# Performance work log

Measured on AMD Instinct MI355X. Metric: run time of the kernel, lower is better.

## Reference

```python
import math
import jax, jax.numpy as jnp
import numpy as np

HID = 4096      # hidden_size
NH = 32         # num_attention_heads
HD = HID // NH  # head_dim = 128
EDGE = 24       # image_edge
K = 12          # pool_kernel_size
PE = 1 + EDGE - K  # pooled_edge = 13
VT = EDGE * EDGE   # vision_tokens = 576
OFF = 5         # image token offset
SR = 2          # scale_ratio


def setup_inputs() -> dict:
    key = jax.random.key(0)
    k1, k2, k3 = jax.random.split(key, 3)
    B, S = 2, 1024
    hidden_states = jax.random.normal(k1, (B, S, HID), jnp.float32)
    W_in = jax.random.normal(k2, (HID, HID), jnp.float32) * 0.02   # input_proj.weight [out,in]
    W_up = jax.random.normal(k3, (HD * SR * SR, HD), jnp.float32) * 0.02  # up_proj.weight [out,in]
    return {"hidden_states": hidden_states, "W_in": W_in, "W_up": W_up}


def reference(hidden_states, W_in, W_up):
    B, S, _ = hidden_states.shape
    residual = hidden_states
    # [B, NH, S, HD] (q and k are identical views of hidden_states)
    qk = hidden_states.reshape(B, S, NH, HD).transpose(0, 2, 1, 3)
    attn = jnp.einsum('bhqd,bhkd->bhqk', qk, qk) / math.sqrt(HD)
    # additive mask applied along the QUERY dim (faithful to original broadcast)
    mask = jnp.zeros((S,), attn.dtype).at[OFF:OFF + VT].set(jnp.finfo(attn.dtype).min)
    attn = attn + mask[None, None, :, None]
    attn = jax.nn.softmax(attn.astype(jnp.float32), axis=-1).astype(qk.dtype)
    attn = attn.sum(axis=2)                        # [B, NH, S]
    image_attn = attn[:, :, OFF:OFF + VT]          # [B, NH, 576]
    image_states = qk[:, :, OFF:OFF + VT, :].reshape(B, NH, EDGE, EDGE, HD)
    ia_soft = jax.nn.softmax(image_attn, axis=-1).reshape(B, NH, EDGE, EDGE)
    ia = image_attn.reshape(B, NH, EDGE, EDGE)
    # AvgPool2d(kernel=12, stride=1) -> [B, NH, 13, 13]
    pooled = jax.lax.reduce_window(ia, 0.0, jax.lax.add,
                                   (1, 1, K, K), (1, 1, 1, 1), 'VALID') / (K * K)
    idx = jnp.argmax(pooled.reshape(B, NH, -1), axis=-1)   # [B, NH]
    row = idx // PE
    col = idx % PE

    def per_head(sm, st, r, c):
        w = jax.lax.dynamic_slice(sm, (r, c), (K, K)).sum()
        win = jax.lax.dynamic_slice(st, (r, c, 0), (K, K, HD))
        return w, win

    # vmap over batch and heads; traced dynamic-slice starts replace the python loops
    w, win = jax.vmap(jax.vmap(per_head))(ia_soft, image_states, row, col)
    up = jnp.einsum('bhijd,ed->bhije', win, W_up)
    # pixel-shuffle back to 24x24 (transpose(3,4) in torch view order)
    up = up.reshape(B, NH, K, K, SR, SR, HD).transpose(0, 1, 2, 4, 3, 5, 6)
    up = up.reshape(B, NH, VT, HD) * w[:, :, None, None]
    img = up.transpose(0, 2, 1, 3).reshape(B, VT, HID)
    hs = jnp.concatenate([hidden_states[:, :OFF], img, hidden_states[:, OFF + VT:]], axis=1)
    hs = jax.nn.silu(hs @ W_in.T)
    return residual + hs
```

## Files before the change

kernel.cpp:

```cpp
#include <hip/hip_runtime.h>
#include <hip/hip_bf16.h>
#include <math.h>

#define HID 4096
#define NH 32
#define HD 128
#define EDGE 24
#define KW 12
#define PEW 13
#define VT 576
#define OFF 5
#define NB 2
#define SLEN 1024
#define QT 64
#define NQT 7
#define KT 64
#define NKT 16

typedef short bf16x8 __attribute__((ext_vector_type(8)));
typedef float f32x4 __attribute__((ext_vector_type(4)));
typedef unsigned int u32;

static __device__ __forceinline__ unsigned short f2bf(float f) {
  union { float f; u32 u; } v; v.f = f;
  u32 u = v.u;
  return (unsigned short)((u + 0x7fffu + ((u >> 16) & 1u)) >> 16);
}

static __device__ __forceinline__ float dot4(float4 a, float4 b) {
  return a.x * b.x + a.y * b.y + a.z * b.z + a.w * b.w;
}

static __device__ __forceinline__ void load_lds16(const void* g, void* l) {
  __builtin_amdgcn_global_load_lds((const __attribute__((address_space(1))) u32*)g,
                                   (__attribute__((address_space(3))) u32*)l, 16, 0, 0);
}

__global__ __launch_bounds__(256) void k_cvt(const float* __restrict__ in,
                                             unsigned short* __restrict__ out, int n4) {
  int i = blockIdx.x * 256 + threadIdx.x;
  if (i < n4) {
    float4 v = ((const float4*)in)[i];
    ushort4 o;
    o.x = f2bf(v.x); o.y = f2bf(v.y); o.z = f2bf(v.z); o.w = f2bf(v.w);
    ((ushort4*)out)[i] = o;
  }
}

__global__ __launch_bounds__(256) void k_pack(const float* __restrict__ hid,
                                              unsigned short* __restrict__ Phi,
                                              unsigned short* __restrict__ Plo) {
  int i = blockIdx.x * 256 + threadIdx.x;
  float4 x = ((const float4*)hid)[i];
  float e[4] = {x.x, x.y, x.z, x.w};
  ushort4 hv, lv;
  unsigned short* hp = (unsigned short*)&hv;
  unsigned short* lp = (unsigned short*)&lv;
#pragma unroll
  for (int j = 0; j < 4; ++j) {
    u32 u = __float_as_uint(e[j]);
    u32 hb = (u + 0x7fffu + ((u >> 16) & 1u)) >> 16;
    float r = e[j] - __uint_as_float(hb << 16);
    u32 ur = __float_as_uint(r);
    u32 lb = (ur + 0x7fffu + ((ur >> 16) & 1u)) >> 16;
    hp[j] = (unsigned short)hb;
    lp[j] = (unsigned short)lb;
  }
  ((ushort4*)Phi)[i] = hv;
  ((ushort4*)Plo)[i] = lv;
}

__global__ __launch_bounds__(512, 2) void k_scores(const unsigned short* __restrict__ Phi,
                                                   const unsigned short* __restrict__ Plo,
                                                   float* __restrict__ part) {
  __shared__ unsigned short Kh[3][KT * HD];
  __shared__ unsigned short Kl[3][KT * HD];
  __shared__ float cs[4][SLEN];
  __shared__ float zbuf[2][QT];

  int bid = blockIdx.x;
  int xcd = bid & 7, idx = bid >> 3;
  int bh = xcd * 8 + idx / NQT;
  int qt = idx % NQT;
  int b = bh >> 5, h = bh & 31;
  int t = threadIdx.x, l = t & 63, wv = t >> 6;
  int wq = wv >> 1, wk = wv & 1;

  const unsigned short* PhB = Phi + (size_t)b * SLEN * HID + h * HD;
  const unsigned short* PlB = Plo + (size_t)b * SLEN * HID + h * HD;

  bf16x8 qhi[4], qlo[4];
  {
    int ql = qt * QT + wq * 16 + (l & 15);
    int qg = (ql < OFF) ? ql : ql + VT;
    const unsigned short* ph = PhB + (size_t)qg * HID + (l >> 4) * 8;
    const unsigned short* pl = PlB + (size_t)qg * HID + (l >> 4) * 8;
#pragma unroll
    for (int ds = 0; ds < 4; ++ds) {
      qhi[ds] = *(const bf16x8*)(ph + ds * 32);
      qlo[ds] = *(const bf16x8*)(pl + ds * 32);
    }
  }

  int g0 = t, g1 = t + 512;
  int r0 = g0 >> 4, r1 = g1 >> 4;
  size_t soff0 = (size_t)r0 * HID + ((g0 & 15) ^ (r0 & 7)) * 8;
  size_t soff1 = (size_t)r1 * HID + ((g1 & 15) ^ (r1 & 7)) * 8;

#define STAGE(kt_, bb_)                                                        \
  do {                                                                         \
    size_t kb_ = (size_t)(kt_)*KT * HID;                                       \
    load_lds16(PhB + kb_ + soff0, &Kh[bb_][g0 * 8]);                           \
    load_lds16(PhB + kb_ + soff1, &Kh[bb_][g1 * 8]);                           \
    load_lds16(PlB + kb_ + soff0, &Kl[bb_][g0 * 8]);                           \
    load_lds16(PlB + kb_ + soff1, &Kl[bb_][g1 * 8]);                           \
  } while (0)

  const float scale = 0.088388347648318447f;

  int foff[2][4];
#pragma unroll
  for (int c = 0; c < 2; ++c) {
    int rb = wk * 32 + c * 16 + (l & 15);
#pragma unroll
    for (int ds = 0; ds < 4; ++ds)
      foff[c][ds] = rb * HD + (((ds * 4) + (l >> 4)) ^ (rb & 7)) * 8;
  }

  float e[NKT][2][4];

  STAGE(0, 0);
  STAGE(1, 1);

#pragma unroll
  for (int tt = 0; tt < NKT; ++tt) {
    int bb = tt % 3;
    if (tt < NKT - 1) {
      asm volatile("s_waitcnt vmcnt(4)" ::: "memory");
    } else {
      asm volatile("s_waitcnt vmcnt(0)" ::: "memory");
    }
    __builtin_amdgcn_s_barrier();
    __builtin_amdgcn_sched_barrier(0);

    bf16x8 kh[2][4], kl[2][4];
#pragma unroll
    for (int c = 0; c < 2; ++c)
#pragma unroll
      for (int ds = 0; ds < 4; ++ds) {
        kh[c][ds] = *(const bf16x8*)&Kh[bb][foff[c][ds]];
        kl[c][ds] = *(const bf16x8*)&Kl[bb][foff[c][ds]];
      }
    if (tt + 2 < NKT) STAGE(tt + 2, (tt + 2) % 3);

#pragma unroll
    for (int c = 0; c < 2; ++c) {
      f32x4 aP = {0.f, 0.f, 0.f, 0.f};
      f32x4 aQ = {0.f, 0.f, 0.f, 0.f};
      f32x4 aR = {0.f, 0.f, 0.f, 0.f};
#pragma unroll
      for (int ds = 0; ds < 4; ++ds) {
        aP = __builtin_amdgcn_mfma_f32_16x16x32_bf16(qhi[ds], kh[c][ds], aP, 0, 0, 0);
        aQ = __builtin_amdgcn_mfma_f32_16x16x32_bf16(qhi[ds], kl[c][ds], aQ, 0, 0, 0);
        aR = __builtin_amdgcn_mfma_f32_16x16x32_bf16(qlo[ds], kh[c][ds], aR, 0, 0, 0);
      }
#pragma unroll
      for (int jj = 0; jj < 4; ++jj)
        e[tt][c][jj] = __expf((aP[jj] + aQ[jj] + aR[jj]) * scale);
    }
  }
#undef STAGE

  float zr[4] = {0.f, 0.f, 0.f, 0.f};
#pragma unroll
  for (int tt = 0; tt < NKT; ++tt)
#pragma unroll
    for (int c = 0; c < 2; ++c)
#pragma unroll
      for (int jj = 0; jj < 4; ++jj) zr[jj] += e[tt][c][jj];
#pragma unroll
  for (int jj = 0; jj < 4; ++jj) {
    float z = zr[jj];
    z += __shfl_xor(z, 1);
    z += __shfl_xor(z, 2);
    z += __shfl_xor(z, 4);
    z += __shfl_xor(z, 8);
    zr[jj] = z;
  }
  if ((l & 15) == 0) {
#pragma unroll
    for (int jj = 0; jj < 4; ++jj)
      zbuf[wk][wq * 16 + (l >> 4) * 4 + jj] = zr[jj];
  }
  __syncthreads();

  float zinv[4];
#pragma unroll
  for (int jj = 0; jj < 4; ++jj) {
    int row = wq * 16 + (l >> 4) * 4 + jj;
    zinv[jj] = 1.f / (zbuf[0][row] + zbuf[1][row]);
  }

#pragma unroll
  for (int tt = 0; tt < NKT; ++tt)
#pragma unroll
    for (int c = 0; c < 2; ++c) {
      float v = e[tt][c][0] * zinv[0] + e[tt][c][1] * zinv[1] +
                e[tt][c][2] * zinv[2] + e[tt][c][3] * zinv[3];
      v += __shfl_xor(v, 16);
      v += __shfl_xor(v, 32);
      if (l < 16) cs[wq][tt * KT + wk * 32 + c * 16 + l] = v;
    }
  __syncthreads();

  for (int c5 = t; c5 < VT; c5 += 512) {
    int col = OFF + c5;
    part[((size_t)bh * NQT + qt) * VT + c5] =
        (cs[0][col] + cs[1][col]) + (cs[2][col] + cs[3][col]);
  }
}

__global__ __launch_bounds__(256) void k_head(const float* __restrict__ part,
                                              float* __restrict__ params) {
  int bh = blockIdx.x;
  int t = threadIdx.x;
  __shared__ float ia[VT];
  __shared__ float sfe[VT];
  __shared__ float rbuf[256];
  __shared__ int ribuf[256];

  for (int i = t; i < VT; i += 256) {
    float s = 0.f;
    const float* p = part + (size_t)bh * NQT * VT + i;
    for (int c = 0; c < NQT; ++c) s += p[(size_t)c * VT];
    ia[i] = s;
  }
  __syncthreads();

  float lm = -1e30f;
  for (int i = t; i < VT; i += 256) lm = fmaxf(lm, ia[i]);
  rbuf[t] = lm;
  __syncthreads();
  for (int s = 128; s > 0; s >>= 1) {
    if (t < s) rbuf[t] = fmaxf(rbuf[t], rbuf[t + s]);
    __syncthreads();
  }
  float M = rbuf[0];
  __syncthreads();

  float lz = 0.f;
  for (int i = t; i < VT; i += 256) {
    float e = __expf(ia[i] - M);
    sfe[i] = e;
    lz += e;
  }
  rbuf[t] = lz;
  __syncthreads();
  for (int s = 128; s > 0; s >>= 1) {
    if (t < s) rbuf[t] += rbuf[t + s];
    __syncthreads();
  }
  float invZ = 1.f / rbuf[0];
  __syncthreads();

  float pv = -1e30f;
  int pidx = 0x7fffffff;
  if (t < PEW * PEW) {
    int r = t / PEW, c = t % PEW;
    float s = 0.f;
    for (int i = 0; i < KW; ++i)
      for (int j = 0; j < KW; ++j) s += ia[(r + i) * EDGE + (c + j)];
    pv = s;
    pidx = t;
  }
  rbuf[t] = pv;
  ribuf[t] = pidx;
  __syncthreads();
  for (int s = 128; s > 0; s >>= 1) {
    if (t < s) {
      float ov = rbuf[t + s];
      int oi = ribuf[t + s];
      if (ov > rbuf[t] || (ov == rbuf[t] && oi < ribuf[t])) {
        rbuf[t] = ov;
        ribuf[t] = oi;
      }
    }
    __syncthreads();
  }
  int idx = ribuf[0];
  int r0 = idx / PEW, c0 = idx % PEW;
  __syncthreads();

  float lw = 0.f;
  if (t < KW * KW) {
    int i = t / KW, j = t % KW;
    lw = sfe[(r0 + i) * EDGE + (c0 + j)];
  }
  rbuf[t] = lw;
  __syncthreads();
  for (int s = 128; s > 0; s >>= 1) {
    if (t < s) rbuf[t] += rbuf[t + s];
    __syncthreads();
  }
  if (t == 0) {
    params[bh * 4 + 0] = rbuf[0] * invZ;
    ((int*)params)[bh * 4 + 1] = r0;
    ((int*)params)[bh * 4 + 2] = c0;
  }
}

__global__ __launch_bounds__(256) void k_img(const float* __restrict__ hid,
                                             const float* __restrict__ Wup,
                                             const float* __restrict__ params,
                                             unsigned short* __restrict__ hs) {
  int bid = blockIdx.x;
  int g = bid & 3;
  int bh = bid >> 2;
  int b = bh / NH, h = bh % NH;
  float w = params[bh * 4];
  int r0 = ((const int*)params)[bh * 4 + 1];
  int c0 = ((const int*)params)[bh * 4 + 2];
  int t = threadIdx.x;

  __shared__ float win[36][HD];
  for (int idx = t; idx < 36 * (HD / 4); idx += 256) {
    int cell = idx >> 5;
    int c4 = idx & 31;
    int cc = g * 36 + cell;
    int i = cc / 12, j = cc % 12;
    int s = OFF + (r0 + i) * EDGE + (c0 + j);
    *(float4*)&win[cell][c4 * 4] =
        *(const float4*)(hid + ((size_t)(b * SLEN + s)) * HID + h * HD + c4 * 4);
  }
  __syncthreads();

  float acc0[36], acc1[36];
#pragma unroll
  for (int cell = 0; cell < 36; ++cell) { acc0[cell] = 0.f; acc1[cell] = 0.f; }

  int e0 = t, e1 = t + 256;
  const float* w0 = Wup + (size_t)e0 * HD;
  const float* w1 = Wup + (size_t)e1 * HD;
  for (int c = 0; c < 32; ++c) {
    float4 u0 = *(const float4*)(w0 + c * 4);
    float4 u1 = *(const float4*)(w1 + c * 4);
#pragma unroll
    for (int cell = 0; cell < 36; ++cell) {
      float4 qv = *(const float4*)&win[cell][c * 4];
      acc0[cell] += dot4(qv, u0);
      acc1[cell] += dot4(qv, u1);
    }
  }

  int si0 = e0 >> 8, sj0 = (e0 >> 7) & 1, d0 = e0 & 127;
  int si1 = e1 >> 8, sj1 = (e1 >> 7) & 1, d1 = e1 & 127;
#pragma unroll
  for (int cell = 0; cell < 36; ++cell) {
    int cc = g * 36 + cell;
    int i = cc / 12, j = cc % 12;
    {
      int srow = OFF + (2 * i + si0) * EDGE + (2 * j + sj0);
      hs[((size_t)(b * SLEN + srow)) * HID + h * HD + d0] = f2bf(acc0[cell] * w);
    }
    {
      int srow = OFF + (2 * i + si1) * EDGE + (2 * j + sj1);
      hs[((size_t)(b * SLEN + srow)) * HID + h * HD + d1] = f2bf(acc1[cell] * w);
    }
  }
}

__global__ __launch_bounds__(512, 2) void k_gemm(const unsigned short* __restrict__ A,
                                                 const unsigned short* __restrict__ Bm,
                                                 const float* __restrict__ resid,
                                                 float* __restrict__ out) {
  __shared__ unsigned short lA[3][128 * 64];
  __shared__ unsigned short lB[3][256 * 64];

  int bid0 = blockIdx.x;
  int swz = (bid0 & 7) * 32 + (bid0 >> 3);
  int bm0 = (swz & 15) << 7;
  int bn0 = (swz >> 4) << 8;
  int t = threadIdx.x;
  int ln = t & 63, wv = t >> 6;
  int wr = wv >> 2, wc = wv & 3;

  int aOff[4][2], bOff[4][2];
#pragma unroll
  for (int q = 0; q < 4; ++q)
#pragma unroll
    for (int ks = 0; ks < 2; ++ks) {
      int ga = ks * 4 + (ln >> 4);
      int ra = wr * 64 + q * 16 + (ln & 15);
      aOff[q][ks] = ra * 64 + ((ga ^ (ra & 7)) * 8);
      int rb = wc * 64 + q * 16 + (ln & 15);
      bOff[q][ks] = rb * 64 + ((ga ^ (rb & 7)) * 8);
    }

  const unsigned short* aS0; const unsigned short* aS1;
  unsigned short *aD0, *aD1;
  {
    int G = t, r = G >> 3, g = G & 7;
    aS0 = A + (size_t)(bm0 + r) * HID + ((g ^ (r & 7)) * 8);
    aD0 = &lA[0][0] + G * 8;
    G = t + 512; r = G >> 3; g = G & 7;
    aS1 = A + (size_t)(bm0 + r) * HID + ((g ^ (r & 7)) * 8);
    aD1 = &lA[0][0] + G * 8;
  }
  const unsigned short *bS0, *bS1, *bS2, *bS3;
  unsigned short *bD0, *bD1, *bD2, *bD3;
  {
    int G = t, r = G >> 3, g = G & 7;
    bS0 = Bm + (size_t)(bn0 + r) * HID + ((g ^ (r & 7)) * 8);
    bD0 = &lB[0][0] + G * 8;
    G = t + 512; r = G >> 3; g = G & 7;
    bS1 = Bm + (size_t)(bn0 + r) * HID + ((g ^ (r & 7)) * 8);
    bD1 = &lB[0][0] + G * 8;
    G = t + 1024; r = G >> 3; g = G & 7;
    bS2 = Bm + (size_t)(bn0 + r) * HID + ((g ^ (r & 7)) * 8);
    bD2 = &lB[0][0] + G * 8;
    G = t + 1536; r = G >> 3; g = G & 7;
    bS3 = Bm + (size_t)(bn0 + r) * HID + ((g ^ (r & 7)) * 8);
    bD3 = &lB[0][0] + G * 8;
  }

#define STAGE_ALL(kt_, nb_)                                \
  load_lds16(aS0 + (kt_) * 64, aD0 + (nb_) * 8192);        \
  load_lds16(aS1 + (kt_) * 64, aD1 + (nb_) * 8192);        \
  load_lds16(bS0 + (kt_) * 64, bD0 + (nb_) * 16384);       \
  load_lds16(bS1 + (kt_) * 64, bD1 + (nb_) * 16384);       \
  load_lds16(bS2 + (kt_) * 64, bD2 + (nb_) * 16384);       \
  load_lds16(bS3 + (kt_) * 64, bD3 + (nb_) * 16384);

  f32x4 acc[4][4];
#pragma unroll
  for (int mi = 0; mi < 4; ++mi)
#pragma unroll
    for (int ni = 0; ni < 4; ++ni) acc[mi][ni] = (f32x4){0.f, 0.f, 0.f, 0.f};

  STAGE_ALL(0, 0);
  STAGE_ALL(1, 1);

  int cur = 0;
  for (int kt = 0; kt < 64; ++kt) {
    if (kt < 63) {
      asm volatile("s_waitcnt vmcnt(6)" ::: "memory");
    } else {
      asm volatile("s_waitcnt vmcnt(0)" ::: "memory");
    }
    __builtin_amdgcn_s_barrier();
    __builtin_amdgcn_sched_barrier(0);

    const unsigned short* Ab = &lA[0][0] + cur * 8192;
    const unsigned short* Bb = &lB[0][0] + cur * 16384;

    bf16x8 aF[4][2], bF[4][2];
#pragma unroll
    for (int q = 0; q < 4; ++q) {
      aF[q][0] = *(const bf16x8*)(Ab + aOff[q][0]);
      aF[q][1] = *(const bf16x8*)(Ab + aOff[q][1]);
      bF[q][0] = *(const bf16x8*)(Bb + bOff[q][0]);
      bF[q][1] = *(const bf16x8*)(Bb + bOff[q][1]);
    }

    int nb = cur + 2; if (nb >= 3) nb -= 3;
    if (kt < 62) { STAGE_ALL(kt + 2, nb); }

    __builtin_amdgcn_s_setprio(1);
#pragma unroll
    for (int ni = 0; ni < 4; ++ni)
#pragma unroll
      for (int mi = 0; mi < 4; ++mi) {
        acc[mi][ni] = __builtin_amdgcn_mfma_f32_16x16x32_bf16(aF[mi][0], bF[ni][0],
                                                              acc[mi][ni], 0, 0, 0);
        acc[mi][ni] = __builtin_amdgcn_mfma_f32_16x16x32_bf16(aF[mi][1], bF[ni][1],
                                                              acc[mi][ni], 0, 0, 0);
      }
    __builtin_amdgcn_s_setprio(0);

    cur = cur + 1; if (cur >= 3) cur = 0;
  }
#undef STAGE_ALL

#pragma unroll
  for (int mi = 0; mi < 4; ++mi) {
#pragma unroll
    for (int ni = 0; ni < 4; ++ni) {
      int m = bm0 + wr * 64 + mi * 16 + (ln >> 4) * 4;
      int n = bn0 + wc * 64 + ni * 16 + (ln & 15);
#pragma unroll
      for (int r = 0; r < 4; ++r) {
        float x = acc[mi][ni][r];
        float s = x / (1.f + __expf(-x));
        size_t o = (size_t)(m + r) * HID + n;
        out[o] = resid[o] + s;
      }
    }
  }
}

extern "C" void kernel_launch(void* const* d_in, const int* in_sizes, int n_in,
                              void* d_out, int out_size, void* d_ws, size_t ws_size,
                              hipStream_t stream) {
  const float* hid = (const float*)d_in[0];
  const float* Win = (const float*)d_in[1];
  const float* Wup = (const float*)d_in[2];
  float* out = (float*)d_out;
  char* ws = (char*)d_ws;

  unsigned short* Wb  = (unsigned short*)ws;
  unsigned short* Phi = (unsigned short*)(ws + 33554432);
  float* part = (float*)(ws + 50331648);
  float* params = (float*)(ws + 52396032);
  unsigned short* Plo = (unsigned short*)d_out;

  k_cvt<<<16384, 256, 0, stream>>>(Win, Wb, HID * HID / 4);
  k_pack<<<NB * SLEN * HID / 4 / 256, 256, 0, stream>>>(hid, Phi, Plo);
  k_scores<<<448, 512, 0, stream>>>(Phi, Plo, part);
  k_head<<<NB * NH, 256, 0, stream>>>(part, params);
  k_img<<<NB * NH * 4, 256, 0, stream>>>(hid, Wup, params, Phi);
  k_gemm<<<256, 512, 0, stream>>>(Phi, Wb, hid, out);
}
```

Measured before the change: 193.6 us.

## Fuse fp32 weight conversion into GEMM loads and switch to 32x32 MFMA

Removes the separate W_in fp32-to-bf16 conversion kernel. The GEMM now loads fp32 weight rows into registers, converts them, and writes swizzled bf16 into LDS one stage ahead, double-buffered through register sets. The MFMA tiling also moves from 16x16x32 to 32x32x16 instructions, with new fragment offsets and epilogue indexing. This saves a full pass over the 64MB weight, but each of the 8 M-tile blocks sharing a weight tile now re-reads it in fp32, doubling weight traffic inside the GEMM and adding VALU conversion and register pressure to the main loop.

```diff
diff --git a/kernel.cpp b/kernel.cpp
--- a/kernel.cpp
+++ b/kernel.cpp
@@ -19,6 +19,7 @@
 
 typedef short bf16x8 __attribute__((ext_vector_type(8)));
 typedef float f32x4 __attribute__((ext_vector_type(4)));
+typedef float f32x16 __attribute__((ext_vector_type(16)));
 typedef unsigned int u32;
 
 static __device__ __forceinline__ unsigned short f2bf(float f) {
@@ -34,17 +35,6 @@
 static __device__ __forceinline__ void load_lds16(const void* g, void* l) {
   __builtin_amdgcn_global_load_lds((const __attribute__((address_space(1))) u32*)g,
                                    (__attribute__((address_space(3))) u32*)l, 16, 0, 0);
-}
-
-__global__ __launch_bounds__(256) void k_cvt(const float* __restrict__ in,
-                                             unsigned short* __restrict__ out, int n4) {
-  int i = blockIdx.x * 256 + threadIdx.x;
-  if (i < n4) {
-    float4 v = ((const float4*)in)[i];
-    ushort4 o;
-    o.x = f2bf(v.x); o.y = f2bf(v.y); o.z = f2bf(v.z); o.w = f2bf(v.w);
-    ((ushort4*)out)[i] = o;
-  }
 }
 
 __global__ __launch_bounds__(256) void k_pack(const float* __restrict__ hid,
@@ -370,7 +360,7 @@
 }
 
 __global__ __launch_bounds__(512, 2) void k_gemm(const unsigned short* __restrict__ A,
-                                                 const unsigned short* __restrict__ Bm,
+                                                 const float* __restrict__ Wf,
                                                  const float* __restrict__ resid,
                                                  float* __restrict__ out) {
   __shared__ unsigned short lA[3][128 * 64];
@@ -384,19 +374,20 @@
   int ln = t & 63, wv = t >> 6;
   int wr = wv >> 2, wc = wv & 3;
 
-  int aOff[4][2], bOff[4][2];
-#pragma unroll
-  for (int q = 0; q < 4; ++q)
-#pragma unroll
-    for (int ks = 0; ks < 2; ++ks) {
-      int ga = ks * 4 + (ln >> 4);
-      int ra = wr * 64 + q * 16 + (ln & 15);
-      aOff[q][ks] = ra * 64 + ((ga ^ (ra & 7)) * 8);
-      int rb = wc * 64 + q * 16 + (ln & 15);
-      bOff[q][ks] = rb * 64 + ((ga ^ (rb & 7)) * 8);
-    }
-
-  const unsigned short* aS0; const unsigned short* aS1;
+  int aOff[2][4], bOff[2][4];
+#pragma unroll
+  for (int mf = 0; mf < 2; ++mf) {
+    int ra = wr * 64 + mf * 32 + (ln & 31);
+    int rb = wc * 64 + mf * 32 + (ln & 31);
+#pragma unroll
+    for (int ks = 0; ks < 4; ++ks) {
+      int g = ks * 2 + (ln >> 5);
+      aOff[mf][ks] = ra * 64 + ((g ^ (ra & 7)) * 8);
+      bOff[mf][ks] = rb * 64 + ((g ^ (rb & 7)) * 8);
+    }
+  }
+
+  const unsigned short *aS0, *aS1;
   unsigned short *aD0, *aD1;
   {
     int G = t, r = G >> 3, g = G & 7;
@@ -406,92 +397,106 @@
     aS1 = A + (size_t)(bm0 + r) * HID + ((g ^ (r & 7)) * 8);
     aD1 = &lA[0][0] + G * 8;
   }
-  const unsigned short *bS0, *bS1, *bS2, *bS3;
-  unsigned short *bD0, *bD1, *bD2, *bD3;
-  {
-    int G = t, r = G >> 3, g = G & 7;
-    bS0 = Bm + (size_t)(bn0 + r) * HID + ((g ^ (r & 7)) * 8);
-    bD0 = &lB[0][0] + G * 8;
-    G = t + 512; r = G >> 3; g = G & 7;
-    bS1 = Bm + (size_t)(bn0 + r) * HID + ((g ^ (r & 7)) * 8);
-    bD1 = &lB[0][0] + G * 8;
-    G = t + 1024; r = G >> 3; g = G & 7;
-    bS2 = Bm + (size_t)(bn0 + r) * HID + ((g ^ (r & 7)) * 8);
-    bD2 = &lB[0][0] + G * 8;
-    G = t + 1536; r = G >> 3; g = G & 7;
-    bS3 = Bm + (size_t)(bn0 + r) * HID + ((g ^ (r & 7)) * 8);
-    bD3 = &lB[0][0] + G * 8;
-  }
-
-#define STAGE_ALL(kt_, nb_)                                \
-  load_lds16(aS0 + (kt_) * 64, aD0 + (nb_) * 8192);        \
-  load_lds16(aS1 + (kt_) * 64, aD1 + (nb_) * 8192);        \
-  load_lds16(bS0 + (kt_) * 64, bD0 + (nb_) * 16384);       \
-  load_lds16(bS1 + (kt_) * 64, bD1 + (nb_) * 16384);       \
-  load_lds16(bS2 + (kt_) * 64, bD2 + (nb_) * 16384);       \
-  load_lds16(bS3 + (kt_) * 64, bD3 + (nb_) * 16384);
-
-  f32x4 acc[4][4];
-#pragma unroll
-  for (int mi = 0; mi < 4; ++mi)
-#pragma unroll
-    for (int ni = 0; ni < 4; ++ni) acc[mi][ni] = (f32x4){0.f, 0.f, 0.f, 0.f};
-
-  STAGE_ALL(0, 0);
-  STAGE_ALL(1, 1);
+
+  int rB = t >> 1;
+  int ch = t & 1;
+  const float* bSrc = Wf + (size_t)(bn0 + rB) * HID + ch * 32;
+  int bWoff[4];
+#pragma unroll
+  for (int w = 0; w < 4; ++w) {
+    int gg = ch * 4 + w;
+    bWoff[w] = rB * 64 + ((gg ^ (rB & 7)) * 8);
+  }
+
+  float4 brE[8], brO[8];
+
+#define LOADB(REGS_, KT_)                                                      \
+  _Pragma("unroll") for (int j = 0; j < 8; ++j)                                \
+      REGS_[j] = *(const float4*)(bSrc + (size_t)(KT_)*64 + j * 4);
+
+#define ISSUE_A(KT_, NB_)                                                      \
+  load_lds16(aS0 + (size_t)(KT_)*64, aD0 + (size_t)(NB_)*8192);                \
+  load_lds16(aS1 + (size_t)(KT_)*64, aD1 + (size_t)(NB_)*8192);
+
+#define CVTW(REGS_, NB_)                                                       \
+  {                                                                            \
+    unsigned short* dst_ = &lB[0][0] + (size_t)(NB_)*16384;                    \
+    _Pragma("unroll") for (int w = 0; w < 4; ++w) {                            \
+      float4 x0_ = REGS_[2 * w], x1_ = REGS_[2 * w + 1];                       \
+      bf16x8 v_;                                                               \
+      v_[0] = (short)f2bf(x0_.x); v_[1] = (short)f2bf(x0_.y);                  \
+      v_[2] = (short)f2bf(x0_.z); v_[3] = (short)f2bf(x0_.w);                  \
+      v_[4] = (short)f2bf(x1_.x); v_[5] = (short)f2bf(x1_.y);                  \
+      v_[6] = (short)f2bf(x1_.z); v_[7] = (short)f2bf(x1_.w);                  \
+      *(bf16x8*)(dst_ + bWoff[w]) = v_;                                        \
+    }                                                                          \
+  }
+
+  f32x16 acc[2][2];
+#pragma unroll
+  for (int mf = 0; mf < 2; ++mf)
+#pragma unroll
+    for (int nf = 0; nf < 2; ++nf)
+#pragma unroll
+      for (int r = 0; r < 16; ++r) acc[mf][nf][r] = 0.f;
+
+  ISSUE_A(0, 0); LOADB(brE, 0);
+  ISSUE_A(1, 1); LOADB(brO, 1);
+  CVTW(brE, 0);
+  asm volatile("s_waitcnt lgkmcnt(0)" ::: "memory");
+  __builtin_amdgcn_s_barrier();
+  __builtin_amdgcn_sched_barrier(0);
 
   int cur = 0;
-  for (int kt = 0; kt < 64; ++kt) {
-    if (kt < 63) {
-      asm volatile("s_waitcnt vmcnt(6)" ::: "memory");
-    } else {
-      asm volatile("s_waitcnt vmcnt(0)" ::: "memory");
-    }
-    __builtin_amdgcn_s_barrier();
-    __builtin_amdgcn_sched_barrier(0);
-
-    const unsigned short* Ab = &lA[0][0] + cur * 8192;
-    const unsigned short* Bb = &lB[0][0] + cur * 16384;
-
-    bf16x8 aF[4][2], bF[4][2];
-#pragma unroll
-    for (int q = 0; q < 4; ++q) {
-      aF[q][0] = *(const bf16x8*)(Ab + aOff[q][0]);
-      aF[q][1] = *(const bf16x8*)(Ab + aOff[q][1]);
-      bF[q][0] = *(const bf16x8*)(Bb + bOff[q][0]);
-      bF[q][1] = *(const bf16x8*)(Bb + bOff[q][1]);
-    }
-
-    int nb = cur + 2; if (nb >= 3) nb -= 3;
-    if (kt < 62) { STAGE_ALL(kt + 2, nb); }
-
-    __builtin_amdgcn_s_setprio(1);
-#pragma unroll
-    for (int ni = 0; ni < 4; ++ni)
-#pragma unroll
-      for (int mi = 0; mi < 4; ++mi) {
-        acc[mi][ni] = __builtin_amdgcn_mfma_f32_16x16x32_bf16(aF[mi][0], bF[ni][0],
-                                                              acc[mi][ni], 0, 0, 0);
-        acc[mi][ni] = __builtin_amdgcn_mfma_f32_16x16x32_bf16(aF[mi][1], bF[ni][1],
-                                                              acc[mi][ni], 0, 0, 0);
-      }
-    __builtin_amdgcn_s_setprio(0);
-
-    cur = cur + 1; if (cur >= 3) cur = 0;
-  }
-#undef STAGE_ALL
-
-#pragma unroll
-  for (int mi = 0; mi < 4; ++mi) {
-#pragma unroll
-    for (int ni = 0; ni < 4; ++ni) {
-      int m = bm0 + wr * 64 + mi * 16 + (ln >> 4) * 4;
-      int n = bn0 + wc * 64 + ni * 16 + (ln & 15);
-#pragma unroll
-      for (int r = 0; r < 4; ++r) {
-        float x = acc[mi][ni][r];
+#define TILE(KT_, BISS_, BCVT_)                                                \
+  {                                                                            \
+    const unsigned short* Ab_ = &lA[0][0] + (size_t)cur * 8192;                \
+    const unsigned short* Bb_ = &lB[0][0] + (size_t)cur * 16384;               \
+    int nb_ = cur + 2; if (nb_ >= 3) nb_ -= 3;                                 \
+    int nb1_ = cur + 1; if (nb1_ >= 3) nb1_ -= 3;                              \
+    bf16x8 aF[2][4], bF[2][4];                                                 \
+    _Pragma("unroll") for (int ks = 0; ks < 4; ++ks) {                         \
+      aF[0][ks] = *(const bf16x8*)(Ab_ + aOff[0][ks]);                         \
+      aF[1][ks] = *(const bf16x8*)(Ab_ + aOff[1][ks]);                         \
+      bF[0][ks] = *(const bf16x8*)(Bb_ + bOff[0][ks]);                         \
+      bF[1][ks] = *(const bf16x8*)(Bb_ + bOff[1][ks]);                         \
+    }                                                                          \
+    if ((KT_) < 62) { ISSUE_A((KT_) + 2, nb_); LOADB(BISS_, (KT_) + 2); }      \
+    if ((KT_) < 63) { CVTW(BCVT_, nb1_); }                                     \
+    __builtin_amdgcn_s_setprio(1);                                             \
+    _Pragma("unroll") for (int ks = 0; ks < 4; ++ks) {                         \
+      acc[0][0] = __builtin_amdgcn_mfma_f32_32x32x16_bf16(aF[0][ks], bF[0][ks], acc[0][0], 0, 0, 0); \
+      acc[0][1] = __builtin_amdgcn_mfma_f32_32x32x16_bf16(aF[0][ks], bF[1][ks], acc[0][1], 0, 0, 0); \
+      acc[1][0] = __builtin_amdgcn_mfma_f32_32x32x16_bf16(aF[1][ks], bF[0][ks], acc[1][0], 0, 0, 0); \
+      acc[1][1] = __builtin_amdgcn_mfma_f32_32x32x16_bf16(aF[1][ks], bF[1][ks], acc[1][1], 0, 0, 0); \
+    }                                                                          \
+    __builtin_amdgcn_s_setprio(0);                                             \
+    asm volatile("s_waitcnt lgkmcnt(0)" ::: "memory");                         \
+    __builtin_amdgcn_s_barrier();                                              \
+    __builtin_amdgcn_sched_barrier(0);                                         \
+    cur = cur + 1; if (cur >= 3) cur = 0;                                      \
+  }
+
+  for (int kt2 = 0; kt2 < 64; kt2 += 2) {
+    TILE(kt2, brE, brO);
+    TILE(kt2 + 1, brO, brE);
+  }
+#undef TILE
+#undef CVTW
+#undef ISSUE_A
+#undef LOADB
+
+#pragma unroll
+  for (int mf = 0; mf < 2; ++mf) {
+#pragma unroll
+    for (int nf = 0; nf < 2; ++nf) {
+      int n = bn0 + wc * 64 + nf * 32 + (ln & 31);
+#pragma unroll
+      for (int r = 0; r < 16; ++r) {
+        int m = bm0 + wr * 64 + mf * 32 + ((r & 3) + 8 * (r >> 2) + 4 * (ln >> 5));
+        float x = acc[mf][nf][r];
         float s = x / (1.f + __expf(-x));
-        size_t o = (size_t)(m + r) * HID + n;
+        size_t o = (size_t)m * HID + n;
         out[o] = resid[o] + s;
       }
     }
@@ -507,16 +512,14 @@
   float* out = (float*)d_out;
   char* ws = (char*)d_ws;
 
-  unsigned short* Wb  = (unsigned short*)ws;
   unsigned short* Phi = (unsigned short*)(ws + 33554432);
   float* part = (float*)(ws + 50331648);
   float* params = (float*)(ws + 52396032);
   unsigned short* Plo = (unsigned short*)d_out;
 
-  k_cvt<<<16384, 256, 0, stream>>>(Win, Wb, HID * HID / 4);
   k_pack<<<NB * SLEN * HID / 4 / 256, 256, 0, stream>>>(hid, Phi, Plo);
   k_scores<<<448, 512, 0, stream>>>(Phi, Plo, part);
   k_head<<<NB * NH, 256, 0, stream>>>(part, params);
   k_img<<<NB * NH * 4, 256, 0, stream>>>(hid, Wup, params, Phi);
-  k_gemm<<<256, 512, 0, stream>>>(Phi, Wb, hid, out);
-}
+  k_gemm<<<256, 512, 0, stream>>>(Phi, Win, hid, out);
+}
```

Result: slower. 255.4 us (+31.9%).
